# Kernel tuning notes

Measured on AMD Instinct MI355X. Metric: run time of the kernel, lower is better.

The kernel has to match this reference:

```python
import jax, jax.numpy as jnp
import numpy as np

D_MODEL = 768
N_HEADS = 12
D_K = D_MODEL // N_HEADS

def setup_inputs() -> dict:
    key = jax.random.key(0)
    ks = jax.random.split(key, 9)
    B, S = 4, 2048
    s = 1.0 / np.sqrt(D_MODEL)
    return {
        "x": jax.random.normal(ks[0], (B, S, D_MODEL), dtype=jnp.float32),
        "Wq": jax.random.normal(ks[1], (D_MODEL, D_MODEL), dtype=jnp.float32) * s,
        "bq": jnp.zeros((D_MODEL,), dtype=jnp.float32),
        "Wk": jax.random.normal(ks[2], (D_MODEL, D_MODEL), dtype=jnp.float32) * s,
        "bk": jnp.zeros((D_MODEL,), dtype=jnp.float32),
        "Wv": jax.random.normal(ks[3], (D_MODEL, D_MODEL), dtype=jnp.float32) * s,
        "bv": jnp.zeros((D_MODEL,), dtype=jnp.float32),
        "Wo": jax.random.normal(ks[4], (D_MODEL, D_MODEL), dtype=jnp.float32) * s,
        "bo": jnp.zeros((D_MODEL,), dtype=jnp.float32),
    }

def reference(x, Wq, bq, Wk, bk, Wv, bv, Wo, bo):
    B, S, _ = x.shape
    # projections (nn.Linear: x @ W^T + b; here weights stored as (in, out) so x @ W + b)
    q = x @ Wq + bq
    k = x @ Wk + bk
    v = x @ Wv + bv
    # split heads -> (B, H, S, d_k)
    q = q.reshape(B, S, N_HEADS, D_K).transpose(0, 2, 1, 3)
    k = k.reshape(B, S, N_HEADS, D_K).transpose(0, 2, 1, 3)
    v = v.reshape(B, S, N_HEADS, D_K).transpose(0, 2, 1, 3)
    scores = jnp.einsum('bhqd,bhkd->bhqk', q, k) / jnp.sqrt(jnp.float32(D_K))
    causal = jnp.tril(jnp.ones((S, S), dtype=bool))  # True = keep
    scores = jnp.where(causal, scores, jnp.finfo(scores.dtype).min)
    weights = jax.nn.softmax(scores, axis=-1)  # dropout is identity in eval
    out = jnp.einsum('bhqk,bhkd->bhqd', weights, v)
    out = out.transpose(0, 2, 1, 3).reshape(B, S, D_MODEL)
    return out @ Wo + bo
```

## Files before the change

### kernel.cpp

```cpp
#include <hip/hip_runtime.h>
#include <hip/hip_bf16.h>

#define DM    768
#define HEADS 12
#define DK    64
#define SEQ   2048
#define BATCH 4
#define NE    ((size_t)BATCH * SEQ * DM)
#define KT    12
#define BRICK 8192

typedef short v8s __attribute__((ext_vector_type(8)));
typedef float v4f __attribute__((ext_vector_type(4)));

#define LDS_PTR(p) ((__attribute__((address_space(3))) unsigned int*)(p))
#define GLB_PTR(p) ((const __attribute__((address_space(1))) unsigned int*)(p))

__device__ __forceinline__ unsigned short f2bf(float f) {
    union { float f; unsigned u; } v; v.f = f;
    unsigned r = (v.u + 0x7FFFu + ((v.u >> 16) & 1u)) >> 16;
    return (unsigned short)r;
}
__device__ __forceinline__ unsigned pk2(float a, float b) {
    union { float f; unsigned u; } x, y; x.f = a; y.f = b;
    return (x.u >> 16) | (y.u & 0xFFFF0000u);
}
__device__ __forceinline__ unsigned pk2r(float a, float b) {
    return (unsigned)f2bf(a) | ((unsigned)f2bf(b) << 16);
}
__device__ __forceinline__ float fexp2(float x) {
#if __has_builtin(__builtin_amdgcn_exp2f)
    return __builtin_amdgcn_exp2f(x);
#else
    return __expf(x * 0.69314718056f);
#endif
}

#define QSCALE 0.18033688011112042f

__global__ __launch_bounds__(256)
void cvt_x_kernel(const float* __restrict__ x, unsigned short* __restrict__ xb) {
    const size_t p = ((size_t)blockIdx.x * 256 + threadIdx.x) * 8;
    const int m = (int)(p / DM);
    const int k = (int)(p % DM);
    const float4 a = *(const float4*)(x + p);
    const float4 b = *(const float4*)(x + p + 4);
    v8s o;
    o[0] = (short)f2bf(a.x); o[1] = (short)f2bf(a.y);
    o[2] = (short)f2bf(a.z); o[3] = (short)f2bf(a.w);
    o[4] = (short)f2bf(b.x); o[5] = (short)f2bf(b.y);
    o[6] = (short)f2bf(b.z); o[7] = (short)f2bf(b.w);
    const size_t dst = ((size_t)(m >> 7) * KT + (k >> 6)) * BRICK + (size_t)(m & 127) * 64 + (k & 63);
    *(v8s*)(xb + dst) = o;
}

__global__ __launch_bounds__(256)
void cvt_w_kernel(const float* __restrict__ W0, const float* __restrict__ W1,
                  const float* __restrict__ W2, const float* __restrict__ W3,
                  unsigned short* __restrict__ wt) {
    __shared__ unsigned short T[64][72];
    const int z = blockIdx.z;
    const float* W = (z == 0) ? W0 : (z == 1) ? W1 : (z == 2) ? W2 : W3;
    const float scale = (z == 0) ? QSCALE : 1.0f;
    const int k0 = blockIdx.x * 64, n0 = blockIdx.y * 64;
    const int t = threadIdx.x;
    {
        const int kr = t >> 2;
        const int ns = (t & 3) * 16;
        #pragma unroll
        for (int j = 0; j < 4; ++j) {
            const float4 v = *(const float4*)(W + (size_t)(k0 + kr) * DM + n0 + ns + j * 4);
            T[ns + j * 4 + 0][kr] = f2bf(v.x * scale);
            T[ns + j * 4 + 1][kr] = f2bf(v.y * scale);
            T[ns + j * 4 + 2][kr] = f2bf(v.z * scale);
            T[ns + j * 4 + 3][kr] = f2bf(v.w * scale);
        }
    }
    __syncthreads();
    {
        unsigned short* dst = wt + (size_t)z * DM * DM +
            ((size_t)(n0 >> 7) * KT + (k0 >> 6)) * BRICK + (size_t)(n0 & 64) * 64;
        const int n = t >> 2;
        const int ks = (t & 3) * 16;
        #pragma unroll
        for (int j = 0; j < 2; ++j)
            *(v8s*)(dst + (size_t)n * 64 + ks + j * 8) = *(const v8s*)&T[n][ks + j * 8];
    }
}

__global__ __launch_bounds__(256)
void gemm_qkv_kernel(const unsigned short* __restrict__ xb, const unsigned short* __restrict__ wtbuf,
                     const float* __restrict__ bq, const float* __restrict__ bk,
                     const float* __restrict__ bv,
                     unsigned short* __restrict__ qb, unsigned short* __restrict__ kb,
                     unsigned short* __restrict__ vtb) {
    __shared__ unsigned short smem[32768];
    const int idx = blockIdx.x;
    const int xcd = idx & 7, g = idx >> 3;
    const int mb = xcd + 8 * (g & 7);
    const int yb = g >> 3;
    const int z = yb / 6;
    const int N0 = (yb % 6) * 128;
    const float* bias = (z == 0) ? bq : (z == 1) ? bk : bv;
    const float bscale = (z == 0) ? QSCALE : 1.0f;

    const int t = threadIdx.x;
    const int w = t >> 6, lane = t & 63, quad = lane >> 4, l15 = lane & 15;
    const int wm = w >> 1, wn = w & 1;
    const int M0 = mb * 128;

    const unsigned short* gA = xb + (size_t)mb * (KT * BRICK);
    const unsigned short* gB = wtbuf + (size_t)yb * (KT * BRICK);

    const int r8 = lane >> 3;
    const int c8 = (lane & 7) ^ r8;
    const int goff = r8 * 64 + c8 * 8;
    const int rl = l15 & 7, rh = l15 >> 3;

    v4f acc[4][4];
    #pragma unroll
    for (int i = 0; i < 4; ++i)
        #pragma unroll
        for (int j = 0; j < 4; ++j) acc[i][j] = (v4f){0, 0, 0, 0};

    #pragma unroll
    for (int u = 0; u < 4; ++u) {
        const int win = w * 4 + u;
        __builtin_amdgcn_global_load_lds(GLB_PTR(gA + win * 512 + goff), LDS_PTR(smem + win * 512), 16, 0, 0);
        __builtin_amdgcn_global_load_lds(GLB_PTR(gB + win * 512 + goff), LDS_PTR(smem + 16384 + win * 512), 16, 0, 0);
    }
    __syncthreads();

    for (int kt = 0; kt < KT; ++kt) {
        const int cur = kt & 1;
        if (kt + 1 < KT) {
            const unsigned short* ta = gA + (kt + 1) * BRICK;
            const unsigned short* tb = gB + (kt + 1) * BRICK;
            const int nb = (1 - cur) * 8192;
            #pragma unroll
            for (int u = 0; u < 4; ++u) {
                const int win = w * 4 + u;
                __builtin_amdgcn_global_load_lds(GLB_PTR(ta + win * 512 + goff), LDS_PTR(smem + nb + win * 512), 16, 0, 0);
                __builtin_amdgcn_global_load_lds(GLB_PTR(tb + win * 512 + goff), LDS_PTR(smem + 16384 + nb + win * 512), 16, 0, 0);
            }
        }
        const unsigned short* As = smem + cur * 8192;
        const unsigned short* Bs = smem + 16384 + cur * 8192;
        #pragma unroll
        for (int kc = 0; kc < 2; ++kc) {
            const int cs = ((kc << 2) | quad) ^ rl;
            v8s a[4], b[4];
            #pragma unroll
            for (int i = 0; i < 4; ++i)
                a[i] = *(const v8s*)&As[(wm * 8 + i * 2 + rh) * 512 + rl * 64 + cs * 8];
            #pragma unroll
            for (int j = 0; j < 4; ++j)
                b[j] = *(const v8s*)&Bs[(wn * 8 + j * 2 + rh) * 512 + rl * 64 + cs * 8];
            #pragma unroll
            for (int i = 0; i < 4; ++i)
                #pragma unroll
                for (int j = 0; j < 4; ++j)
                    acc[i][j] = __builtin_amdgcn_mfma_f32_16x16x32_bf16(a[i], b[j], acc[i][j], 0, 0, 0);
        }
        __syncthreads();
    }

    const int b_ = M0 >> 11;
    const int sidx0 = M0 & 2047;
    const int h0 = N0 >> 6;

    if (z < 2) {
        unsigned short* outp = (z == 0) ? qb : kb;
        #pragma unroll
        for (int j = 0; j < 4; ++j) {
            const int n = N0 + wn * 64 + j * 16 + l15;
            const int h = n >> 6, d = n & 63;
            const float bv_ = bias[n] * bscale;
            #pragma unroll
            for (int i = 0; i < 4; ++i)
                #pragma unroll
                for (int r = 0; r < 4; ++r) {
                    const int sidx = sidx0 + wm * 64 + i * 16 + quad * 4 + r;
                    outp[(((size_t)(b_ * HEADS + h) * SEQ + sidx) << 6) + d] = f2bf(acc[i][j][r] + bv_);
                }
        }
    } else {
        unsigned short* Ts = smem;
        #pragma unroll
        for (int p = 0; p < 2; ++p) {
            __syncthreads();
            if (wm == p) {
                #pragma unroll
                for (int j = 0; j < 4; ++j) {
                    const int dloc = wn * 64 + j * 16 + l15;
                    const float bv_ = bias[N0 + dloc];
                    #pragma unroll
                    for (int i = 0; i < 4; ++i)
                        #pragma unroll
                        for (int r = 0; r < 4; ++r)
                            Ts[dloc * 72 + i * 16 + quad * 4 + r] = f2bf(acc[i][j][r] + bv_);
                }
            }
            __syncthreads();
            const int dloc = t >> 1, ms = (t & 1) * 32;
            const int h = h0 + (dloc >> 6), d = dloc & 63;
            unsigned short* dst = vtb + (((size_t)(b_ * HEADS + h) * DK + d) << 11) + sidx0 + p * 64 + ms;
            #pragma unroll
            for (int jj = 0; jj < 4; ++jj)
                *(v8s*)(dst + jj * 8) = *(const v8s*)&Ts[dloc * 72 + ms + jj * 8];
        }
    }
}

__global__ __launch_bounds__(256)
void gemm_out_kernel(const unsigned short* __restrict__ ob, const unsigned short* __restrict__ wto,
                     const float* __restrict__ bias, float* __restrict__ out) {
    __shared__ unsigned short smem[24576];
    const int idx = blockIdx.x;
    const int xcd = idx & 7, g = idx >> 3;
    const int mb = xcd + 8 * (g & 7);
    const int nb = g >> 3;
    const int t = threadIdx.x;
    const int w = t >> 6, lane = t & 63, quad = lane >> 4, l15 = lane & 15;
    const int wm = w >> 1, wn = w & 1;
    const int M0 = mb * 128;
    const int N0 = nb * 64;

    const unsigned short* gA = ob + (size_t)mb * (KT * BRICK);
    const unsigned short* gB = wto + (size_t)(nb >> 1) * (KT * BRICK) + (nb & 1) * 4096;

    const int r8 = lane >> 3;
    const int c8 = (lane & 7) ^ r8;
    const int goff = r8 * 64 + c8 * 8;
    const int rl = l15 & 7, rh = l15 >> 3;

    v4f acc[4][2];
    #pragma unroll
    for (int i = 0; i < 4; ++i)
        #pragma unroll
        for (int j = 0; j < 2; ++j) acc[i][j] = (v4f){0, 0, 0, 0};

    #pragma unroll
    for (int u = 0; u < 4; ++u) {
        const int win = w * 4 + u;
        __builtin_amdgcn_global_load_lds(GLB_PTR(gA + win * 512 + goff), LDS_PTR(smem + win * 512), 16, 0, 0);
    }
    #pragma unroll
    for (int u = 0; u < 2; ++u) {
        const int win = w * 2 + u;
        __builtin_amdgcn_global_load_lds(GLB_PTR(gB + win * 512 + goff), LDS_PTR(smem + 16384 + win * 512), 16, 0, 0);
    }
    __syncthreads();

    for (int kt = 0; kt < KT; ++kt) {
        const int cur = kt & 1;
        if (kt + 1 < KT) {
            const unsigned short* ta = gA + (kt + 1) * BRICK;
            const unsigned short* tb = gB + (kt + 1) * BRICK;
            #pragma unroll
            for (int u = 0; u < 4; ++u) {
                const int win = w * 4 + u;
                __builtin_amdgcn_global_load_lds(GLB_PTR(ta + win * 512 + goff),
                                                 LDS_PTR(smem + (1 - cur) * 8192 + win * 512), 16, 0, 0);
            }
            #pragma unroll
            for (int u = 0; u < 2; ++u) {
                const int win = w * 2 + u;
                __builtin_amdgcn_global_load_lds(GLB_PTR(tb + win * 512 + goff),
                                                 LDS_PTR(smem + 16384 + (1 - cur) * 4096 + win * 512), 16, 0, 0);
            }
        }
        const unsigned short* As = smem + cur * 8192;
        const unsigned short* Bs = smem + 16384 + cur * 4096;
        #pragma unroll
        for (int kc = 0; kc < 2; ++kc) {
            const int cs = ((kc << 2) | quad) ^ rl;
            v8s a[4], b[2];
            #pragma unroll
            for (int i = 0; i < 4; ++i)
                a[i] = *(const v8s*)&As[(wm * 8 + i * 2 + rh) * 512 + rl * 64 + cs * 8];
            #pragma unroll
            for (int j = 0; j < 2; ++j)
                b[j] = *(const v8s*)&Bs[(wn * 4 + j * 2 + rh) * 512 + rl * 64 + cs * 8];
            #pragma unroll
            for (int i = 0; i < 4; ++i)
                #pragma unroll
                for (int j = 0; j < 2; ++j)
                    acc[i][j] = __builtin_amdgcn_mfma_f32_16x16x32_bf16(a[i], b[j], acc[i][j], 0, 0, 0);
        }
        __syncthreads();
    }

    #pragma unroll
    for (int j = 0; j < 2; ++j) {
        const int n = N0 + wn * 32 + j * 16 + l15;
        const float bv_ = bias[n];
        #pragma unroll
        for (int i = 0; i < 4; ++i)
            #pragma unroll
            for (int r = 0; r < 4; ++r) {
                const int m = M0 + wm * 64 + i * 16 + quad * 4 + r;
                out[(size_t)m * DM + n] = acc[i][j][r] + bv_;
            }
    }
}

__global__ __launch_bounds__(256, 4)
void attn_kernel(const unsigned short* __restrict__ Q, const unsigned short* __restrict__ K,
                 const unsigned short* __restrict__ VT, unsigned short* __restrict__ O) {
    __shared__ unsigned short Kb[2][64][64];
    __shared__ unsigned short Vb[2][64][64];
    __shared__ unsigned short Ps[4][16][64];
    const int t = threadIdx.x;
    const int w = t >> 6, lane = t & 63, quad = lane >> 4, l15 = lane & 15;
    const int e7 = l15 & 7;

    const int idx = blockIdx.x;
    const int xcd = idx & 7;
    const int g   = idx >> 3;
    const int bh  = xcd + 8 * (g % 6);
    const int s   = 31 - g / 6;
    const int q0  = s * 64;
    const int nkt = s + 1;
    const size_t kvbase = (size_t)bh * SEQ * DK;

    v8s qf[2];
    #pragma unroll
    for (int c = 0; c < 2; ++c)
        qf[c] = *(const v8s*)(Q + kvbase + (size_t)(q0 + w * 16 + l15) * DK + c * 32 + quad * 8);

    v4f o[4];
    #pragma unroll
    for (int nf = 0; nf < 4; ++nf) o[nf] = (v4f){0, 0, 0, 0};
    v4f os = (v4f){0, 0, 0, 0};
    const v4f zero4 = (v4f){0, 0, 0, 0};

    const short one_bf = (short)0x3F80;
    const v8s ones = (v8s){one_bf, one_bf, one_bf, one_bf, one_bf, one_bf, one_bf, one_bf};

    const int srow = t >> 3;
    const int sc16 = t & 7;
    const int scolsw = (sc16 ^ (srow & 7)) * 8;
    const int gcol = sc16 * 8;

    v8s kr0 = *(const v8s*)(K  + kvbase + (size_t)srow * DK + gcol);
    v8s kr1 = *(const v8s*)(K  + kvbase + (size_t)(srow + 32) * DK + gcol);
    v8s vr0 = *(const v8s*)(VT + kvbase + ((size_t)srow << 11) + gcol);
    v8s vr1 = *(const v8s*)(VT + kvbase + ((size_t)(srow + 32) << 11) + gcol);
    *(v8s*)&Kb[0][srow][scolsw]      = kr0;
    *(v8s*)&Kb[0][srow + 32][scolsw] = kr1;
    *(v8s*)&Vb[0][srow][scolsw]      = vr0;
    *(v8s*)&Vb[0][srow + 32][scolsw] = vr1;
    __syncthreads();

    const int q_ = q0 + w * 16 + l15;

    for (int kt = 0; kt < nkt; ++kt) {
        const int k0 = kt * 64;
        const int cur = kt & 1;
        if (kt + 1 < nkt) {
            const int kn = k0 + 64;
            kr0 = *(const v8s*)(K  + kvbase + (size_t)(kn + srow) * DK + gcol);
            kr1 = *(const v8s*)(K  + kvbase + (size_t)(kn + srow + 32) * DK + gcol);
            vr0 = *(const v8s*)(VT + kvbase + ((size_t)srow << 11) + kn + gcol);
            vr1 = *(const v8s*)(VT + kvbase + ((size_t)(srow + 32) << 11) + kn + gcol);
        }

        v4f sc[4];
        #pragma unroll
        for (int s4 = 0; s4 < 4; ++s4) {
            const v8s kf = *(const v8s*)&Kb[cur][s4 * 16 + l15][(quad ^ e7) * 8];
            sc[s4] = __builtin_amdgcn_mfma_f32_16x16x32_bf16(kf, qf[0], zero4, 0, 0, 0);
        }
        #pragma unroll
        for (int s4 = 0; s4 < 4; ++s4) {
            const v8s kf = *(const v8s*)&Kb[cur][s4 * 16 + l15][((4 | quad) ^ e7) * 8];
            sc[s4] = __builtin_amdgcn_mfma_f32_16x16x32_bf16(kf, qf[1], sc[s4], 0, 0, 0);
        }

        {
            const bool msk = (kt == s);
            #pragma unroll
            for (int s4 = 0; s4 < 4; ++s4) {
                float p[4];
                #pragma unroll
                for (int r = 0; r < 4; ++r) p[r] = fexp2(sc[s4][r]);
                if (msk) {
                    #pragma unroll
                    for (int r = 0; r < 4; ++r) {
                        const int key = k0 + s4 * 16 + quad * 4 + r;
                        if (key > q_) p[r] = 0.f;
                    }
                }
                uint2 pkv; pkv.x = pk2(p[0], p[1]); pkv.y = pk2(p[2], p[3]);
                const int col8 = (s4 * 4 + quad) ^ (e7 << 1);
                *(uint2*)&Ps[w][l15][col8 * 4] = pkv;
            }
        }

        #pragma unroll
        for (int kc = 0; kc < 2; ++kc) {
            const int c16 = ((kc * 4 + quad) ^ e7) * 8;
            const v8s pf = *(const v8s*)&Ps[w][l15][c16];
            os = __builtin_amdgcn_mfma_f32_16x16x32_bf16(ones, pf, os, 0, 0, 0);
            #pragma unroll
            for (int nf = 0; nf < 4; ++nf) {
                const v8s vf = *(const v8s*)&Vb[cur][nf * 16 + l15][c16];
                o[nf] = __builtin_amdgcn_mfma_f32_16x16x32_bf16(vf, pf, o[nf], 0, 0, 0);
            }
        }

        if (kt + 1 < nkt) {
            const int nxt = 1 - cur;
            *(v8s*)&Kb[nxt][srow][scolsw]      = kr0;
            *(v8s*)&Kb[nxt][srow + 32][scolsw] = kr1;
            *(v8s*)&Vb[nxt][srow][scolsw]      = vr0;
            *(v8s*)&Vb[nxt][srow + 32][scolsw] = vr1;
        }
        __syncthreads();
    }

    const float inv = 1.f / os[0];

    const int b = bh / HEADS, h = bh % HEADS;
    const size_t br = ((size_t)(b * 16 + (q0 >> 7)) * KT + h) * BRICK;
    const int rowl = (q0 & 127) + w * 16 + l15;
    #pragma unroll
    for (int nf = 0; nf < 4; ++nf) {
        uint2 a2;
        a2.x = pk2r(o[nf][0] * inv, o[nf][1] * inv);
        a2.y = pk2r(o[nf][2] * inv, o[nf][3] * inv);
        *(uint2*)(O + br + (size_t)rowl * 64 + nf * 16 + quad * 4) = a2;
    }
}

extern "C" void kernel_launch(void* const* d_in, const int* in_sizes, int n_in,
                              void* d_out, int out_size, void* d_ws, size_t ws_size,
                              hipStream_t stream) {
    const float* x  = (const float*)d_in[0];
    const float* Wq = (const float*)d_in[1];
    const float* bq = (const float*)d_in[2];
    const float* Wk = (const float*)d_in[3];
    const float* bk = (const float*)d_in[4];
    const float* Wv = (const float*)d_in[5];
    const float* bv = (const float*)d_in[6];
    const float* Wo = (const float*)d_in[7];
    const float* bo = (const float*)d_in[8];
    float* out = (float*)d_out;

    unsigned short* xb  = (unsigned short*)d_ws;
    unsigned short* qb  = xb  + NE;
    unsigned short* kb  = qb  + NE;
    unsigned short* vtb = kb  + NE;
    unsigned short* wt  = vtb + NE;
    unsigned short* ob  = xb;

    cvt_x_kernel<<<dim3(NE / (8 * 256)), 256, 0, stream>>>(x, xb);
    cvt_w_kernel<<<dim3(12, 12, 4), 256, 0, stream>>>(Wq, Wk, Wv, Wo, wt);
    gemm_qkv_kernel<<<dim3(1152), 256, 0, stream>>>(xb, wt, bq, bk, bv, qb, kb, vtb);
    attn_kernel<<<dim3(1536), 256, 0, stream>>>(qb, kb, vtb, ob);
    gemm_out_kernel<<<dim3(768), 256, 0, stream>>>(ob, wt + (size_t)3 * DM * DM, bo, out);
}
```

Baseline: 189.5 us.

## Pair short and long causal query tiles per block to share K/V loads

Each attention block now handles two query tiles, p and 31-p, so every block does the same total causal work, and the short tile reuses the K/V tiles already staged in shared memory for the long one. The grid is halved and the V fragments loaded from LDS are kept in registers and reused for both tiles. This is meant to balance load across blocks and cut redundant K/V global and LDS traffic. In exchange it raises register pressure (launch bounds lowered to 3 waves per SIMD) and doubles the P staging buffer.

New measurement: 192.4 us. No clear change (+1.5%).

```diff
diff --git a/kernel.cpp b/kernel.cpp
--- a/kernel.cpp
+++ b/kernel.cpp
@@ -305,12 +305,13 @@
     }
 }
 
-__global__ __launch_bounds__(256, 4)
+__global__ __launch_bounds__(256, 3)
 void attn_kernel(const unsigned short* __restrict__ Q, const unsigned short* __restrict__ K,
                  const unsigned short* __restrict__ VT, unsigned short* __restrict__ O) {
     __shared__ unsigned short Kb[2][64][64];
     __shared__ unsigned short Vb[2][64][64];
-    __shared__ unsigned short Ps[4][16][64];
+    __shared__ unsigned short PsA[4][16][64];
+    __shared__ unsigned short PsB[4][16][64];
     const int t = threadIdx.x;
     const int w = t >> 6, lane = t & 63, quad = lane >> 4, l15 = lane & 15;
     const int e7 = l15 & 7;
@@ -319,20 +320,23 @@
     const int xcd = idx & 7;
     const int g   = idx >> 3;
     const int bh  = xcd + 8 * (g % 6);
-    const int s   = 31 - g / 6;
-    const int q0  = s * 64;
-    const int nkt = s + 1;
+    const int p   = g / 6;
+    const int sA  = p, sB = 31 - p;
+    const int q0A = sA * 64, q0B = sB * 64;
+    const int nkt = sB + 1;
     const size_t kvbase = (size_t)bh * SEQ * DK;
 
-    v8s qf[2];
-    #pragma unroll
-    for (int c = 0; c < 2; ++c)
-        qf[c] = *(const v8s*)(Q + kvbase + (size_t)(q0 + w * 16 + l15) * DK + c * 32 + quad * 8);
-
-    v4f o[4];
-    #pragma unroll
-    for (int nf = 0; nf < 4; ++nf) o[nf] = (v4f){0, 0, 0, 0};
-    v4f os = (v4f){0, 0, 0, 0};
+    v8s qfA[2], qfB[2];
+    #pragma unroll
+    for (int c = 0; c < 2; ++c) {
+        qfA[c] = *(const v8s*)(Q + kvbase + (size_t)(q0A + w * 16 + l15) * DK + c * 32 + quad * 8);
+        qfB[c] = *(const v8s*)(Q + kvbase + (size_t)(q0B + w * 16 + l15) * DK + c * 32 + quad * 8);
+    }
+
+    v4f oA[4], oB[4];
+    #pragma unroll
+    for (int nf = 0; nf < 4; ++nf) { oA[nf] = (v4f){0,0,0,0}; oB[nf] = (v4f){0,0,0,0}; }
+    v4f osA = (v4f){0, 0, 0, 0}, osB = (v4f){0, 0, 0, 0};
     const v4f zero4 = (v4f){0, 0, 0, 0};
 
     const short one_bf = (short)0x3F80;
@@ -353,7 +357,8 @@
     *(v8s*)&Vb[0][srow + 32][scolsw] = vr1;
     __syncthreads();
 
-    const int q_ = q0 + w * 16 + l15;
+    const int qA = q0A + w * 16 + l15;
+    const int qB = q0B + w * 16 + l15;
 
     for (int kt = 0; kt < nkt; ++kt) {
         const int k0 = kt * 64;
@@ -366,47 +371,81 @@
             vr1 = *(const v8s*)(VT + kvbase + ((size_t)(srow + 32) << 11) + kn + gcol);
         }
 
-        v4f sc[4];
+        const bool actA = (kt <= sA);
+
+        v4f scA[4], scB[4];
         #pragma unroll
         for (int s4 = 0; s4 < 4; ++s4) {
             const v8s kf = *(const v8s*)&Kb[cur][s4 * 16 + l15][(quad ^ e7) * 8];
-            sc[s4] = __builtin_amdgcn_mfma_f32_16x16x32_bf16(kf, qf[0], zero4, 0, 0, 0);
+            scB[s4] = __builtin_amdgcn_mfma_f32_16x16x32_bf16(kf, qfB[0], zero4, 0, 0, 0);
+            if (actA) scA[s4] = __builtin_amdgcn_mfma_f32_16x16x32_bf16(kf, qfA[0], zero4, 0, 0, 0);
         }
         #pragma unroll
         for (int s4 = 0; s4 < 4; ++s4) {
             const v8s kf = *(const v8s*)&Kb[cur][s4 * 16 + l15][((4 | quad) ^ e7) * 8];
-            sc[s4] = __builtin_amdgcn_mfma_f32_16x16x32_bf16(kf, qf[1], sc[s4], 0, 0, 0);
+            scB[s4] = __builtin_amdgcn_mfma_f32_16x16x32_bf16(kf, qfB[1], scB[s4], 0, 0, 0);
+            if (actA) scA[s4] = __builtin_amdgcn_mfma_f32_16x16x32_bf16(kf, qfA[1], scA[s4], 0, 0, 0);
         }
 
         {
-            const bool msk = (kt == s);
+            const bool msk = (kt == nkt - 1);
             #pragma unroll
             for (int s4 = 0; s4 < 4; ++s4) {
-                float p[4];
-                #pragma unroll
-                for (int r = 0; r < 4; ++r) p[r] = fexp2(sc[s4][r]);
+                float pv[4];
+                #pragma unroll
+                for (int r = 0; r < 4; ++r) pv[r] = fexp2(scB[s4][r]);
                 if (msk) {
                     #pragma unroll
                     for (int r = 0; r < 4; ++r) {
                         const int key = k0 + s4 * 16 + quad * 4 + r;
-                        if (key > q_) p[r] = 0.f;
+                        if (key > qB) pv[r] = 0.f;
                     }
                 }
-                uint2 pkv; pkv.x = pk2(p[0], p[1]); pkv.y = pk2(p[2], p[3]);
+                uint2 pkv; pkv.x = pk2(pv[0], pv[1]); pkv.y = pk2(pv[2], pv[3]);
                 const int col8 = (s4 * 4 + quad) ^ (e7 << 1);
-                *(uint2*)&Ps[w][l15][col8 * 4] = pkv;
-            }
-        }
-
+                *(uint2*)&PsB[w][l15][col8 * 4] = pkv;
+            }
+        }
+
+        v8s vfc[2][4];
         #pragma unroll
         for (int kc = 0; kc < 2; ++kc) {
             const int c16 = ((kc * 4 + quad) ^ e7) * 8;
-            const v8s pf = *(const v8s*)&Ps[w][l15][c16];
-            os = __builtin_amdgcn_mfma_f32_16x16x32_bf16(ones, pf, os, 0, 0, 0);
+            const v8s pf = *(const v8s*)&PsB[w][l15][c16];
+            osB = __builtin_amdgcn_mfma_f32_16x16x32_bf16(ones, pf, osB, 0, 0, 0);
             #pragma unroll
             for (int nf = 0; nf < 4; ++nf) {
-                const v8s vf = *(const v8s*)&Vb[cur][nf * 16 + l15][c16];
-                o[nf] = __builtin_amdgcn_mfma_f32_16x16x32_bf16(vf, pf, o[nf], 0, 0, 0);
+                vfc[kc][nf] = *(const v8s*)&Vb[cur][nf * 16 + l15][c16];
+                oB[nf] = __builtin_amdgcn_mfma_f32_16x16x32_bf16(vfc[kc][nf], pf, oB[nf], 0, 0, 0);
+            }
+        }
+
+        if (actA) {
+            const bool msk = (kt == sA);
+            #pragma unroll
+            for (int s4 = 0; s4 < 4; ++s4) {
+                float pv[4];
+                #pragma unroll
+                for (int r = 0; r < 4; ++r) pv[r] = fexp2(scA[s4][r]);
+                if (msk) {
+                    #pragma unroll
+                    for (int r = 0; r < 4; ++r) {
+                        const int key = k0 + s4 * 16 + quad * 4 + r;
+                        if (key > qA) pv[r] = 0.f;
+                    }
+                }
+                uint2 pkv; pkv.x = pk2(pv[0], pv[1]); pkv.y = pk2(pv[2], pv[3]);
+                const int col8 = (s4 * 4 + quad) ^ (e7 << 1);
+                *(uint2*)&PsA[w][l15][col8 * 4] = pkv;
+            }
+            #pragma unroll
+            for (int kc = 0; kc < 2; ++kc) {
+                const int c16 = ((kc * 4 + quad) ^ e7) * 8;
+                const v8s pf = *(const v8s*)&PsA[w][l15][c16];
+                osA = __builtin_amdgcn_mfma_f32_16x16x32_bf16(ones, pf, osA, 0, 0, 0);
+                #pragma unroll
+                for (int nf = 0; nf < 4; ++nf)
+                    oA[nf] = __builtin_amdgcn_mfma_f32_16x16x32_bf16(vfc[kc][nf], pf, oA[nf], 0, 0, 0);
             }
         }
 
@@ -420,17 +459,22 @@
         __syncthreads();
     }
 
-    const float inv = 1.f / os[0];
+    const float invA = 1.f / osA[0], invB = 1.f / osB[0];
 
     const int b = bh / HEADS, h = bh % HEADS;
-    const size_t br = ((size_t)(b * 16 + (q0 >> 7)) * KT + h) * BRICK;
-    const int rowl = (q0 & 127) + w * 16 + l15;
+    const size_t brA = ((size_t)(b * 16 + (q0A >> 7)) * KT + h) * BRICK;
+    const size_t brB = ((size_t)(b * 16 + (q0B >> 7)) * KT + h) * BRICK;
+    const int rowlA = (q0A & 127) + w * 16 + l15;
+    const int rowlB = (q0B & 127) + w * 16 + l15;
     #pragma unroll
     for (int nf = 0; nf < 4; ++nf) {
-        uint2 a2;
-        a2.x = pk2r(o[nf][0] * inv, o[nf][1] * inv);
-        a2.y = pk2r(o[nf][2] * inv, o[nf][3] * inv);
-        *(uint2*)(O + br + (size_t)rowl * 64 + nf * 16 + quad * 4) = a2;
+        uint2 a2, b2;
+        a2.x = pk2r(oA[nf][0] * invA, oA[nf][1] * invA);
+        a2.y = pk2r(oA[nf][2] * invA, oA[nf][3] * invA);
+        b2.x = pk2r(oB[nf][0] * invB, oB[nf][1] * invB);
+        b2.y = pk2r(oB[nf][2] * invB, oB[nf][3] * invB);
+        *(uint2*)(O + brA + (size_t)rowlA * 64 + nf * 16 + quad * 4) = a2;
+        *(uint2*)(O + brB + (size_t)rowlB * 64 + nf * 16 + quad * 4) = b2;
     }
 }
 
@@ -458,6 +502,6 @@
     cvt_x_kernel<<<dim3(NE / (8 * 256)), 256, 0, stream>>>(x, xb);
     cvt_w_kernel<<<dim3(12, 12, 4), 256, 0, stream>>>(Wq, Wk, Wv, Wo, wt);
     gemm_qkv_kernel<<<dim3(1152), 256, 0, stream>>>(xb, wt, bq, bk, bv, qb, kb, vtb);
-    attn_kernel<<<dim3(1536), 256, 0, stream>>>(qb, kb, vtb, ob);
+    attn_kernel<<<dim3(768), 256, 0, stream>>>(qb, kb, vtb, ob);
     gemm_out_kernel<<<dim3(768), 256, 0, stream>>>(ob, wt + (size_t)3 * DM * DM, bo, out);
 }
```

## Use direct global-to-LDS loads and software-pipeline PV MFMAs in attention

Applied to the files above, without the earlier changes.

The K/V tile prefetch now uses async global_load_lds with a matching XOR swizzle, replacing the global-to-register-to-LDS staging. The P·V MFMA for each tile is deferred by one iteration: V fragments are cached in registers and consumed after the next QK^T, so it can overlap the exp/pack work, with an epilogue handling the last tile. Launch bounds drop from 4 to 3 waves per SIMD to make room for the extra registers. The trade-off is lower occupancy and correctness that depends on the compiler waiting on the async LDS writes before the barrier.

After: 192.9 us, median of 2. About the same (+1.8%).

```diff
diff --git a/kernel.cpp b/kernel.cpp
--- a/kernel.cpp
+++ b/kernel.cpp
@@ -305,7 +305,7 @@
     }
 }
 
-__global__ __launch_bounds__(256, 4)
+__global__ __launch_bounds__(256, 3)
 void attn_kernel(const unsigned short* __restrict__ Q, const unsigned short* __restrict__ K,
                  const unsigned short* __restrict__ VT, unsigned short* __restrict__ O) {
     __shared__ unsigned short Kb[2][64][64];
@@ -338,32 +338,35 @@
     const short one_bf = (short)0x3F80;
     const v8s ones = (v8s){one_bf, one_bf, one_bf, one_bf, one_bf, one_bf, one_bf, one_bf};
 
-    const int srow = t >> 3;
-    const int sc16 = t & 7;
-    const int scolsw = (sc16 ^ (srow & 7)) * 8;
-    const int gcol = sc16 * 8;
-
-    v8s kr0 = *(const v8s*)(K  + kvbase + (size_t)srow * DK + gcol);
-    v8s kr1 = *(const v8s*)(K  + kvbase + (size_t)(srow + 32) * DK + gcol);
-    v8s vr0 = *(const v8s*)(VT + kvbase + ((size_t)srow << 11) + gcol);
-    v8s vr1 = *(const v8s*)(VT + kvbase + ((size_t)(srow + 32) << 11) + gcol);
-    *(v8s*)&Kb[0][srow][scolsw]      = kr0;
-    *(v8s*)&Kb[0][srow + 32][scolsw] = kr1;
-    *(v8s*)&Vb[0][srow][scolsw]      = vr0;
-    *(v8s*)&Vb[0][srow + 32][scolsw] = vr1;
+    const int lrow  = lane >> 3;
+    const int gslot = ((lane & 7) ^ lrow) * 8;
+
+    #pragma unroll
+    for (int u = 0; u < 2; ++u) {
+        const int row = w * 16 + u * 8 + lrow;
+        __builtin_amdgcn_global_load_lds(GLB_PTR(K + kvbase + (size_t)row * DK + gslot),
+                                         LDS_PTR(&Kb[0][w * 16 + u * 8][0]), 16, 0, 0);
+        __builtin_amdgcn_global_load_lds(GLB_PTR(VT + kvbase + ((size_t)row << 11) + gslot),
+                                         LDS_PTR(&Vb[0][w * 16 + u * 8][0]), 16, 0, 0);
+    }
     __syncthreads();
 
     const int q_ = q0 + w * 16 + l15;
+    v8s vfc[2][4];
 
     for (int kt = 0; kt < nkt; ++kt) {
         const int k0 = kt * 64;
         const int cur = kt & 1;
         if (kt + 1 < nkt) {
             const int kn = k0 + 64;
-            kr0 = *(const v8s*)(K  + kvbase + (size_t)(kn + srow) * DK + gcol);
-            kr1 = *(const v8s*)(K  + kvbase + (size_t)(kn + srow + 32) * DK + gcol);
-            vr0 = *(const v8s*)(VT + kvbase + ((size_t)srow << 11) + kn + gcol);
-            vr1 = *(const v8s*)(VT + kvbase + ((size_t)(srow + 32) << 11) + kn + gcol);
+            #pragma unroll
+            for (int u = 0; u < 2; ++u) {
+                const int row = w * 16 + u * 8 + lrow;
+                __builtin_amdgcn_global_load_lds(GLB_PTR(K + kvbase + (size_t)(kn + row) * DK + gslot),
+                                                 LDS_PTR(&Kb[1 - cur][w * 16 + u * 8][0]), 16, 0, 0);
+                __builtin_amdgcn_global_load_lds(GLB_PTR(VT + kvbase + ((size_t)row << 11) + kn + gslot),
+                                                 LDS_PTR(&Vb[1 - cur][w * 16 + u * 8][0]), 16, 0, 0);
+            }
         }
 
         v4f sc[4];
@@ -378,21 +381,33 @@
             sc[s4] = __builtin_amdgcn_mfma_f32_16x16x32_bf16(kf, qf[1], sc[s4], 0, 0, 0);
         }
 
+        if (kt > 0) {
+            #pragma unroll
+            for (int kc = 0; kc < 2; ++kc) {
+                const int c16 = ((kc * 4 + quad) ^ e7) * 8;
+                const v8s pf = *(const v8s*)&Ps[w][l15][c16];
+                os = __builtin_amdgcn_mfma_f32_16x16x32_bf16(ones, pf, os, 0, 0, 0);
+                #pragma unroll
+                for (int nf = 0; nf < 4; ++nf)
+                    o[nf] = __builtin_amdgcn_mfma_f32_16x16x32_bf16(vfc[kc][nf], pf, o[nf], 0, 0, 0);
+            }
+        }
+
         {
             const bool msk = (kt == s);
             #pragma unroll
             for (int s4 = 0; s4 < 4; ++s4) {
-                float p[4];
-                #pragma unroll
-                for (int r = 0; r < 4; ++r) p[r] = fexp2(sc[s4][r]);
+                float pv[4];
+                #pragma unroll
+                for (int r = 0; r < 4; ++r) pv[r] = fexp2(sc[s4][r]);
                 if (msk) {
                     #pragma unroll
                     for (int r = 0; r < 4; ++r) {
                         const int key = k0 + s4 * 16 + quad * 4 + r;
-                        if (key > q_) p[r] = 0.f;
+                        if (key > q_) pv[r] = 0.f;
                     }
                 }
-                uint2 pkv; pkv.x = pk2(p[0], p[1]); pkv.y = pk2(p[2], p[3]);
+                uint2 pkv; pkv.x = pk2(pv[0], pv[1]); pkv.y = pk2(pv[2], pv[3]);
                 const int col8 = (s4 * 4 + quad) ^ (e7 << 1);
                 *(uint2*)&Ps[w][l15][col8 * 4] = pkv;
             }
@@ -401,23 +416,22 @@
         #pragma unroll
         for (int kc = 0; kc < 2; ++kc) {
             const int c16 = ((kc * 4 + quad) ^ e7) * 8;
-            const v8s pf = *(const v8s*)&Ps[w][l15][c16];
-            os = __builtin_amdgcn_mfma_f32_16x16x32_bf16(ones, pf, os, 0, 0, 0);
-            #pragma unroll
-            for (int nf = 0; nf < 4; ++nf) {
-                const v8s vf = *(const v8s*)&Vb[cur][nf * 16 + l15][c16];
-                o[nf] = __builtin_amdgcn_mfma_f32_16x16x32_bf16(vf, pf, o[nf], 0, 0, 0);
-            }
-        }
-
-        if (kt + 1 < nkt) {
-            const int nxt = 1 - cur;
-            *(v8s*)&Kb[nxt][srow][scolsw]      = kr0;
-            *(v8s*)&Kb[nxt][srow + 32][scolsw] = kr1;
-            *(v8s*)&Vb[nxt][srow][scolsw]      = vr0;
-            *(v8s*)&Vb[nxt][srow + 32][scolsw] = vr1;
-        }
+            #pragma unroll
+            for (int nf = 0; nf < 4; ++nf)
+                vfc[kc][nf] = *(const v8s*)&Vb[cur][nf * 16 + l15][c16];
+        }
+
         __syncthreads();
+    }
+
+    #pragma unroll
+    for (int kc = 0; kc < 2; ++kc) {
+        const int c16 = ((kc * 4 + quad) ^ e7) * 8;
+        const v8s pf = *(const v8s*)&Ps[w][l15][c16];
+        os = __builtin_amdgcn_mfma_f32_16x16x32_bf16(ones, pf, os, 0, 0, 0);
+        #pragma unroll
+        for (int nf = 0; nf < 4; ++nf)
+            o[nf] = __builtin_amdgcn_mfma_f32_16x16x32_bf16(vfc[kc][nf], pf, o[nf], 0, 0, 0);
     }
 
     const float inv = 1.f / os[0];
```
